# Kernel optimization log

Hardware: AMD Instinct MI355X
Metric: run time of the kernel (lower is better)

## Reference

```python
import jax, jax.numpy as jnp
import numpy as np

L = 4096   # num_tokens (one prefill sequence)
D = 2048   # hidden_size
HK = 16    # num_k_heads
HV = 32    # num_v_heads
DK = 128   # head_k_dim
DV = 128   # head_v_dim
RATIO = HV // HK
EPS = 1e-6


def setup_inputs() -> dict:
    key = jax.random.key(0)
    ks = jax.random.split(key, 11)
    s = 0.02
    return {
        "hidden_states": jax.random.normal(ks[0], (L, D), jnp.float32),
        "Wq": jax.random.normal(ks[1], (D, HK * DK), jnp.float32) * s,
        "Wk": jax.random.normal(ks[2], (D, HK * DK), jnp.float32) * s,
        "Wv": jax.random.normal(ks[3], (D, HV * DV), jnp.float32) * s,
        "Wz": jax.random.normal(ks[4], (D, HV * DV), jnp.float32) * s,
        "Wb": jax.random.normal(ks[5], (D, HV), jnp.float32) * s,
        "Wa": jax.random.normal(ks[6], (D, HV), jnp.float32) * s,
        "A_log": jnp.log(jax.random.uniform(ks[7], (HV,), jnp.float32, 1.0, 16.0)),
        "dt_bias": jax.random.normal(ks[8], (HV,), jnp.float32) * 0.5,
        "norm_weight": jnp.ones((DV,), jnp.float32),
        "W_out": jax.random.normal(ks[9], (HV * DV, D), jnp.float32) * s,
    }


def _l2norm(x):
    return x * jax.lax.rsqrt(jnp.sum(x * x, axis=-1, keepdims=True) + EPS)


def reference(hidden_states, Wq, Wk, Wv, Wz, Wb, Wa, A_log, dt_bias, norm_weight, W_out):
    h = hidden_states
    # --- input projections (qkvz + ba split) ---
    q = _l2norm((h @ Wq).reshape(L, HK, DK))            # [L, HK, DK]
    k = _l2norm((h @ Wk).reshape(L, HK, DK))
    v = (h @ Wv).reshape(L, HV, DV)                     # [L, HV, DV]
    z = (h @ Wz).reshape(L, HV, DV)                     # gate for RMSNorm
    beta = jax.nn.sigmoid(h @ Wb)                       # [L, HV]
    g = -jnp.exp(A_log) * jax.nn.softplus(h @ Wa + dt_bias)  # [L, HV]
    decay = jnp.exp(g)                                  # per-token per-head decay
    # repeat shared q/k heads to value heads (GQA ratio)
    q = jnp.repeat(q, RATIO, axis=1) * (DK ** -0.5)     # [L, HV, DK]
    k = jnp.repeat(k, RATIO, axis=1)

    # --- gated delta rule recurrence over tokens ---
    def step(S, xs):
        q_t, k_t, v_t, b_t, d_t = xs                    # [HV,DK],[HV,DK],[HV,DV],[HV],[HV]
        S = S * d_t[:, None, None]                      # decay state [HV, DK, DV]
        pred = jnp.einsum('hk,hkv->hv', k_t, S)         # memory readout
        delta = (v_t - pred) * b_t[:, None]             # delta-rule correction
        S = S + k_t[:, :, None] * delta[:, None, :]
        o = jnp.einsum('hk,hkv->hv', q_t, S)
        return S, o

    S0 = jnp.zeros((HV, DK, DV), jnp.float32)
    _, core = jax.lax.scan(step, S0, (q, k, v, beta, decay))  # core: [L, HV, DV]

    # --- gated RMSNorm: x * silu(z), rms-normalize over head dim ---
    x = core * jax.nn.silu(z)
    x = x * jax.lax.rsqrt(jnp.mean(x * x, axis=-1, keepdims=True) + EPS) * norm_weight

    # --- output projection ---
    return x.reshape(L, HV * DV) @ W_out                # [L, D]
```

## Files before the change

kernel.cpp:

```cpp
#include <hip/hip_runtime.h>

#define LTOK 4096
#define DHID 2048
#define HKN  16
#define HVN  32
#define DKK  128
#define NTOT 12288

typedef unsigned short u16;
typedef __attribute__((ext_vector_type(8))) short short8;
typedef __attribute__((ext_vector_type(8))) unsigned short u16x8;
typedef __attribute__((ext_vector_type(4))) unsigned short u16x4;
typedef __attribute__((ext_vector_type(4))) float f32x4;

__device__ __forceinline__ float b2f(u16 u) {
  unsigned int x = ((unsigned int)u) << 16;
  return __builtin_bit_cast(float, x);
}
__device__ __forceinline__ u16 f2bf(float f) {
  unsigned int u = __builtin_bit_cast(unsigned int, f);
  u += 0x7FFFu + ((u >> 16) & 1u);
  return (u16)(u >> 16);
}

template<int C> __device__ __forceinline__ float dppmv(float x) {
  int i = __builtin_amdgcn_update_dpp(0, __builtin_bit_cast(int, x), C, 0xF, 0xF, true);
  return __builtin_bit_cast(float, i);
}
__device__ __forceinline__ float red16(float x) {
  x += dppmv<0xB1>(x);
  x += dppmv<0x4E>(x);
  x += dppmv<0x124>(x);
  x += dppmv<0x128>(x);
  return x;
}

__device__ __forceinline__ void gld16(const void* g, void* l) {
  __builtin_amdgcn_global_load_lds((const __attribute__((address_space(1))) void*)g,
                                   (__attribute__((address_space(3))) void*)l, 16, 0, 0);
}

template<int OFF> __device__ __forceinline__ short8 dsr(unsigned a) {
  short8 r;
  asm volatile("ds_read_b128 %0, %1 offset:%2" : "=v"(r) : "v"(a), "n"(OFF));
  return r;
}

__device__ __forceinline__ int sw16(int r, int c, int rowc) { return (r * rowc + c) ^ ((r & 7) << 3); }

__device__ __forceinline__ void cstore(u16* C, size_t i, float v) { C[i] = f2bf(v); }
__device__ __forceinline__ void cstore(float* C, size_t i, float v) { C[i] = v; }

__global__ __launch_bounds__(256)
void k_cvt(const float* __restrict__ s, u16* __restrict__ d, int n) {
  const int i = (blockIdx.x * 256 + threadIdx.x) * 4;
  const float4 v = *(const float4*)(s + i);
  ushort4 o;
  o.x = f2bf(v.x); o.y = f2bf(v.y); o.z = f2bf(v.z); o.w = f2bf(v.w);
  *(ushort4*)(d + i) = o;
}

__global__ __launch_bounds__(256)
void k_tr(const float* __restrict__ src, u16* __restrict__ dst, int R, int C) {
  __shared__ float tl[32][33];
  const int r0 = blockIdx.y * 32, c0 = blockIdx.x * 32;
  const int tr = threadIdx.x >> 3, tc = (threadIdx.x & 7) * 4;
  const float4 v = *(const float4*)(src + (size_t)(r0 + tr) * C + c0 + tc);
  tl[tr][tc] = v.x; tl[tr][tc + 1] = v.y; tl[tr][tc + 2] = v.z; tl[tr][tc + 3] = v.w;
  __syncthreads();
  ushort4 o;
  o.x = f2bf(tl[tc + 0][tr]); o.y = f2bf(tl[tc + 1][tr]);
  o.z = f2bf(tl[tc + 2][tr]); o.w = f2bf(tl[tc + 3][tr]);
  *(ushort4*)(dst + (size_t)(c0 + tr) * R + r0 + tc) = o;
}

#define MFMA16(a, b, c) __builtin_amdgcn_mfma_f32_16x16x32_bf16(a, b, c, 0, 0, 0)

template<typename OutT, int NWN>
__global__ __launch_bounds__(512, 2)
void k_g256(const u16* __restrict__ A, const u16* __restrict__ Bt, OutT* __restrict__ C,
            int M, int N, int K, int NT) {
  constexpr int BUFE = 8192 + NWN * 2048;
  constexpr int BN = NWN * 64;
  __shared__ u16 Lds[4 * BUFE];
  const int tid = threadIdx.x;
  const int lane = tid & 63, w = tid >> 6;
  const int fr = lane & 15, fq = lane >> 4;
  const int wm = (w >> 2) * 128, wn = (w & 3) * (NWN * 16);
  const int nkt = K >> 5;
  const size_t sK = (size_t)K;

  const int MT = gridDim.x / NT;
  const int nts = (NT < 16) ? NT : 16;
  const int per_super = MT * nts;
  const int super = blockIdx.x / per_super;
  const int within = blockIdx.x % per_super;
  const int mtg = MT >> 3;
  const int q = within >> 3;
  const int mt = (within & 7) * mtg + (q % mtg);
  const int nt = super * nts + q / mtg;

  const int kslot = ((tid & 3) ^ ((tid >> 3) & 3)) * 8;
  const u16* aS = A + (size_t)(mt * 256 + (tid >> 2)) * sK + kslot;
  const u16* bS = Bt + (size_t)(nt * BN + (tid >> 2)) * sK + kslot;

  f32x4 acc[8][NWN] = {};

  auto STAGE = [&](int kt_) {
    const int sk = (kt_ < nkt) ? kt_ : nkt - 1;
    u16* base = &Lds[(kt_ & 3) * BUFE];
    gld16(aS + (size_t)sk * 32, base + w * 512);
    gld16(aS + 128 * sK + (size_t)sk * 32, base + w * 512 + 4096);
    gld16(bS + (size_t)sk * 32, base + 8192 + w * 512);
    if constexpr (NWN == 4)
      gld16(bS + 128 * sK + (size_t)sk * 32, base + 8192 + w * 512 + 4096);
  };

  STAGE(0); STAGE(1); STAGE(2);

  const int akey = (fr >> 1) & 3;
  const unsigned ldsBase = (unsigned)(size_t)(__attribute__((address_space(3))) void*)&Lds[0];
  const unsigned aA0 = ldsBase + 2u * (unsigned)((wm + fr) * 32 + ((fq ^ akey) << 3));
  const unsigned bA0 = ldsBase + 2u * (unsigned)(8192 + (wn + fr) * 32 + ((fq ^ akey) << 3));

  short8 afA[8], bfA[NWN], afB[8], bfB[NWN];

#define RD(afX, bfX, kt_) {                                                   \
    const unsigned bo = (unsigned)(((kt_) & 3) * BUFE * 2);                   \
    const unsigned aAr = aA0 + bo, bAr = bA0 + bo;                            \
    bfX[0] = dsr<0>(bAr); bfX[1] = dsr<1024>(bAr);                            \
    if constexpr (NWN == 4) { bfX[2] = dsr<2048>(bAr); bfX[3] = dsr<3072>(bAr); } \
    afX[0] = dsr<0>(aAr);    afX[1] = dsr<1024>(aAr);                         \
    afX[2] = dsr<2048>(aAr); afX[3] = dsr<3072>(aAr);                         \
    afX[4] = dsr<4096>(aAr); afX[5] = dsr<5120>(aAr);                         \
    afX[6] = dsr<6144>(aAr); afX[7] = dsr<7168>(aAr); }

  if constexpr (NWN == 4) asm volatile("s_waitcnt vmcnt(8)" ::: "memory");
  else                    asm volatile("s_waitcnt vmcnt(6)" ::: "memory");
  __builtin_amdgcn_s_barrier();
  RD(afA, bfA, 0)
  asm volatile("s_waitcnt lgkmcnt(0)" ::: "memory");
  __builtin_amdgcn_sched_barrier(0);

#define ITER(kt_, afC, bfC, afN, bfN) {                                       \
    STAGE((kt_) + 3);                                                         \
    if constexpr (NWN == 4) asm volatile("s_waitcnt vmcnt(8)" ::: "memory");  \
    else                    asm volatile("s_waitcnt vmcnt(6)" ::: "memory");  \
    __builtin_amdgcn_s_barrier();                                             \
    __builtin_amdgcn_sched_barrier(0);                                        \
    RD(afN, bfN, (kt_) + 1)                                                   \
    __builtin_amdgcn_sched_barrier(0);                                        \
    __builtin_amdgcn_s_setprio(1);                                            \
    _Pragma("unroll")                                                         \
    for (int i = 0; i < 8; ++i)                                               \
      _Pragma("unroll")                                                       \
      for (int j = 0; j < NWN; ++j)                                           \
        acc[i][j] = MFMA16(afC[i], bfC[j], acc[i][j]);                        \
    __builtin_amdgcn_s_setprio(0);                                            \
    asm volatile("s_waitcnt lgkmcnt(0)" ::: "memory");                        \
    __builtin_amdgcn_sched_barrier(0); }

  for (int kt = 0; kt < nkt; kt += 2) {
    ITER(kt, afA, bfA, afB, bfB)
    ITER(kt + 1, afB, bfB, afA, bfA)
  }
#undef ITER
#undef RD

  const int r0 = mt * 256 + wm + fq * 4;
  const int c0 = nt * BN + wn + fr;
#pragma unroll
  for (int i = 0; i < 8; ++i)
#pragma unroll
    for (int j = 0; j < NWN; ++j)
#pragma unroll
      for (int e = 0; e < 4; ++e)
        cstore(C, (size_t)(r0 + i * 16 + e) * N + c0 + j * 16, acc[i][j][e]);
}

__global__ __launch_bounds__(256)
void k_ba(const float* __restrict__ h, const float* __restrict__ Wb, const float* __restrict__ Wa,
          const float* __restrict__ A_log, const float* __restrict__ dtb,
          float* __restrict__ beta, float* __restrict__ g_out) {
  const int w = threadIdx.x >> 6, lane = threadIdx.x & 63;
  const int t = blockIdx.x * 4 + w;
  const int j = lane & 31;
  const bool isB = lane < 32;
  const float* __restrict__ hr = h + (size_t)t * DHID;
  const float* Wc = isB ? Wb : Wa;
  float acc = 0.f;
  for (int kk = 0; kk < DHID; ++kk) acc = fmaf(hr[kk], Wc[(size_t)kk * HVN + j], acc);
  if (isB) {
    beta[(size_t)t * HVN + j] = 1.f / (1.f + expf(-acc));
  } else {
    float xx = acc + dtb[j];
    float sp = (xx > 20.f) ? xx : log1pf(expf(xx));
    g_out[(size_t)t * HVN + j] = -expf(A_log[j]) * sp;
  }
}

__global__ __launch_bounds__(256)
void k_l2n(u16* __restrict__ qkvz) {
  const int w = threadIdx.x >> 6, lane = threadIdx.x & 63;
  const int r = blockIdx.x * 4 + w;
  const int isK = r >> 16;
  const int rr = r & 65535;
  const int t = rr >> 4, hd = rr & 15;
  u16* p = qkvz + (size_t)t * NTOT + isK * 2048 + hd * DKK + lane * 2;
  float a = b2f(p[0]), b = b2f(p[1]);
  float ss = a * a + b * b;
  ss = red16(ss);
  ss += __shfl_xor(ss, 16);
  ss += __shfl_xor(ss, 32);
  const float sc = rsqrtf(ss + 1e-6f) * (isK ? 1.f : 0.08838834764831845f);
  p[0] = f2bf(a * sc); p[1] = f2bf(b * sc);
}

__global__ __launch_bounds__(256)
void k_r1(const u16* __restrict__ qkvz, const float* __restrict__ beta_g,
          const float* __restrict__ g_g, u16* __restrict__ UM_g, float* __restrict__ cumL_g) {
  const int pair = blockIdx.x;
  const int hv = pair >> 6, n = pair & 63;
  const int hk = hv >> 1;
  const int t0 = n * 64;
  const int tid = threadIdx.x, lane = tid & 63, wv = tid >> 6;
  const int fr = lane & 15, fq = lane >> 4;

  __shared__ __align__(16) u16 Xb[256 * 64];
  __shared__ __align__(16) u16 Dbuf0[64 * 64 * 2];
  __shared__ __align__(16) u16 Dbuf1[64 * 64 * 2];
  __shared__ float Lc[64];
  __shared__ float Bc[64];
  u16* Kl = Dbuf0;

  const int j = tid & 63, h = tid >> 6;
  const u16* kg = qkvz + (size_t)(t0 + j) * NTOT + 2048 + hk * DKK + h * 32;
  const u16* vg = qkvz + (size_t)(t0 + j) * NTOT + 4096 + hv * DKK + h * 32;
  u16x8 kv[4], vv[4];
#pragma unroll
  for (int i = 0; i < 4; ++i) { kv[i] = *(const u16x8*)(kg + i * 8); vv[i] = *(const u16x8*)(vg + i * 8); }
  if (tid < 64) {
    Lc[tid] = g_g[(size_t)(t0 + tid) * HVN + hv];
    Bc[tid] = beta_g[(size_t)(t0 + tid) * HVN + hv];
  }
#pragma unroll
  for (int i = 0; i < 4; ++i) *(u16x8*)&Kl[sw16(j, h * 32 + i * 8, 128)] = kv[i];
  __syncthreads();
  if (tid == 0) { float a = 0.f; for (int t = 0; t < 64; ++t) { a += Lc[t]; Lc[t] = a; } }
  __syncthreads();
  if (tid < 64) cumL_g[(size_t)pair * 64 + tid] = Lc[tid];

  {
    const float bj = Bc[j];
    const float mj = bj * __expf(Lc[j]);
#pragma unroll
    for (int i = 0; i < 4; ++i)
#pragma unroll
      for (int e = 0; e < 8; ++e) {
        int c = h * 32 + i * 8 + e;
        Xb[sw16(c, j, 64)] = f2bf(bj * b2f(vv[i][e]));
        Xb[sw16(128 + c, j, 64)] = f2bf(mj * b2f(kv[i][e]));
      }
  }
  f32x4 kk[4] = {};
#pragma unroll
  for (int ks = 0; ks < 4; ++ks) {
    short8 afr = *(const short8*)&Kl[sw16(wv * 16 + fr, ks * 32 + fq * 8, 128)];
#pragma unroll
    for (int ct = 0; ct < 4; ++ct) {
      short8 bfr = *(const short8*)&Kl[sw16(ct * 16 + fr, ks * 32 + fq * 8, 128)];
      kk[ct] = MFMA16(afr, bfr, kk[ct]);
    }
  }
  __syncthreads();

  f32x4 acc[16];
#pragma unroll
  for (int ct = 0; ct < 16; ++ct) {
    u16x4 xi = *(const u16x4*)&Xb[sw16(ct * 16 + fr, wv * 16 + fq * 4, 64)];
    acc[ct][0] = b2f(xi[0]); acc[ct][1] = b2f(xi[1]); acc[ct][2] = b2f(xi[2]); acc[ct][3] = b2f(xi[3]);
  }
#pragma unroll
  for (int ct = 0; ct < 4; ++ct) {
    const int s = ct * 16 + fr;
    u16x4 pk;
#pragma unroll
    for (int e = 0; e < 4; ++e) {
      const int t = wv * 16 + fq * 4 + e;
      float v = (s < t) ? -Bc[t] * __expf(Lc[t] - Lc[s]) * kk[ct][e] : 0.f;
      pk[e] = f2bf(v);
      Dbuf0[sw16(t, s, 64)] = pk[e];
    }
    *(u16x4*)&Dbuf0[4096 + sw16(s, wv * 16 + fq * 4, 64)] = pk;
  }
  __syncthreads();

  u16* DA = Dbuf0;
  u16* DB = Dbuf1;
  for (int stg = 0; stg < 6; ++stg) {
    u16* Dr = DA;
    u16* Dc = DA + 4096;
    short8 da0 = *(const short8*)&Dr[sw16(wv * 16 + fr, 0 + fq * 8, 64)];
    short8 da1 = *(const short8*)&Dr[sw16(wv * 16 + fr, 32 + fq * 8, 64)];
#pragma unroll
    for (int ct = 0; ct < 16; ++ct) {
      short8 b0 = *(const short8*)&Xb[sw16(ct * 16 + fr, 0 + fq * 8, 64)];
      short8 b1 = *(const short8*)&Xb[sw16(ct * 16 + fr, 32 + fq * 8, 64)];
      acc[ct] = MFMA16(da0, b0, acc[ct]);
      acc[ct] = MFMA16(da1, b1, acc[ct]);
    }
    f32x4 sq[4] = {};
    if (stg < 5) {
#pragma unroll
      for (int ct = 0; ct < 4; ++ct) {
        short8 sb0 = *(const short8*)&Dc[sw16(ct * 16 + fr, 0 + fq * 8, 64)];
        short8 sb1 = *(const short8*)&Dc[sw16(ct * 16 + fr, 32 + fq * 8, 64)];
        sq[ct] = MFMA16(da0, sb0, sq[ct]);
        sq[ct] = MFMA16(da1, sb1, sq[ct]);
      }
    }
    __syncthreads();
#pragma unroll
    for (int ct = 0; ct < 16; ++ct) {
      u16x4 pk;
      pk[0] = f2bf(acc[ct][0]); pk[1] = f2bf(acc[ct][1]); pk[2] = f2bf(acc[ct][2]); pk[3] = f2bf(acc[ct][3]);
      *(u16x4*)&Xb[sw16(ct * 16 + fr, wv * 16 + fq * 4, 64)] = pk;
    }
    if (stg < 5) {
#pragma unroll
      for (int ct = 0; ct < 4; ++ct) {
        u16x4 pk;
        pk[0] = f2bf(sq[ct][0]); pk[1] = f2bf(sq[ct][1]); pk[2] = f2bf(sq[ct][2]); pk[3] = f2bf(sq[ct][3]);
        *(u16x4*)&(DB + 4096)[sw16(ct * 16 + fr, wv * 16 + fq * 4, 64)] = pk;
#pragma unroll
        for (int e = 0; e < 4; ++e) DB[sw16(wv * 16 + fq * 4 + e, ct * 16 + fr, 64)] = pk[e];
      }
    }
    __syncthreads();
    u16* tmp = DA; DA = DB; DB = tmp;
  }

#pragma unroll
  for (int ct = 0; ct < 16; ++ct) {
    const int c = ct * 16 + fr;
#pragma unroll
    for (int e = 0; e < 4; ++e) {
      const int t = wv * 16 + fq * 4 + e;
      float v = acc[ct][e];
      if (ct >= 8) v = -v;
      UM_g[((size_t)pair * 64 + t) * 256 + c] = f2bf(v);
    }
  }
}

__global__ __launch_bounds__(512)
void k_r2(u16* __restrict__ qkvz, const u16* __restrict__ UM_g,
          const float* __restrict__ cumL_g, u16* __restrict__ o1_g) {
  const int hv = blockIdx.x >> 2, cs = blockIdx.x & 3;
  const int hk = hv >> 1;
  const int tid = threadIdx.x, lane = tid & 63, w = tid >> 6;
  const int fr = lane & 15, fq = lane >> 4;
  const int j = tid & 63, h = tid >> 6;
  const int tw = w & 3, dwv = w >> 2;

  __shared__ __align__(16) u16 Ml2[2][8192];
  __shared__ __align__(16) u16 Ql2[2][8192];
  __shared__ __align__(16) u16 Kt2[2][8192];
  __shared__ __align__(16) u16 dT[2048];
  __shared__ __align__(16) u16 SbT[4096];
  __shared__ __align__(16) u16 o1b[2048];
  __shared__ float Lc2[2][64];

  f32x4 sacc[2];
#pragma unroll
  for (int d = 0; d < 2; ++d) sacc[d] = (f32x4){0.f, 0.f, 0.f, 0.f};
  for (int i = tid; i < 4096; i += 512) SbT[i] = 0;

  u16x8 pQ0, pQ1, pK0, pK1, pM0, pM1;
  u16 pUn0, pUn1, pUn2, pUn3, pUc0, pUc1, pUc2, pUc3;
  float pL, pL63;

#define PREF(nn) {                                                            \
    const int nc = ((nn) < 64) ? (nn) : 63;                                   \
    const int pr = hv * 64 + nc; const int tt0 = nc * 64;                     \
    const u16* qg = qkvz + (size_t)(tt0 + j) * NTOT + hk * DKK + h * 16;      \
    pQ0 = *(const u16x8*)qg;          pQ1 = *(const u16x8*)(qg + 8);          \
    pK0 = *(const u16x8*)(qg + 2048); pK1 = *(const u16x8*)(qg + 2056);       \
    const u16* mg = UM_g + ((size_t)pr * 64 + j) * 256;                       \
    pM0 = *(const u16x8*)(mg + 128 + h * 16);                                 \
    pM1 = *(const u16x8*)(mg + 136 + h * 16);                                 \
    const u16* ug = UM_g + ((size_t)pr * 64 + tw * 16 + fq * 4) * 256         \
                    + cs * 32 + dwv * 16 + fr;                                \
    pUn0 = ug[0]; pUn1 = ug[256]; pUn2 = ug[512]; pUn3 = ug[768];             \
    pL = cumL_g[(size_t)pr * 64 + j]; pL63 = cumL_g[(size_t)pr * 64 + 63]; }

#define STW(b) {                                                              \
    *(u16x8*)&Ql2[b][sw16(j, h * 16, 128)] = pQ0;                             \
    *(u16x8*)&Ql2[b][sw16(j, h * 16 + 8, 128)] = pQ1;                         \
    *(u16x8*)&Ml2[b][sw16(j, h * 16, 128)] = pM0;                             \
    *(u16x8*)&Ml2[b][sw16(j, h * 16 + 8, 128)] = pM1;                         \
    const float scK = __expf(pL63 - pL);                                      \
    _Pragma("unroll")                                                         \
    for (int e = 0; e < 8; ++e) {                                             \
      Kt2[b][sw16(h * 16 + e, j, 64)] = f2bf(scK * b2f(pK0[e]));              \
      Kt2[b][sw16(h * 16 + 8 + e, j, 64)] = f2bf(scK * b2f(pK1[e]));          \
    }                                                                         \
    if (h == 0) Lc2[b][j] = pL; }

  PREF(0)
  STW(0)
  __syncthreads();

  for (int n = 0; n < 64; ++n) {
    const int cur = n & 1;
    const int pair = hv * 64 + n, t0 = n * 64;
    pUc0 = pUn0; pUc1 = pUn1; pUc2 = pUn2; pUc3 = pUn3;
    const float curL63 = pL63;
    PREF(n + 1)

    short8 amf[4], aqf[4];
#pragma unroll
    for (int ks = 0; ks < 4; ++ks) {
      amf[ks] = *(const short8*)&Ml2[cur][sw16(tw * 16 + fr, ks * 32 + fq * 8, 128)];
      aqf[ks] = *(const short8*)&Ql2[cur][sw16(tw * 16 + fr, ks * 32 + fq * 8, 128)];
    }
    float el[4];
#pragma unroll
    for (int e = 0; e < 4; ++e) el[e] = __expf(Lc2[cur][tw * 16 + fq * 4 + e]);
    {
      f32x4 dc;
      dc[0] = b2f(pUc0); dc[1] = b2f(pUc1); dc[2] = b2f(pUc2); dc[3] = b2f(pUc3);
      f32x4 oc = {};
#pragma unroll
      for (int ks = 0; ks < 4; ++ks) {
        short8 bs = *(const short8*)&SbT[sw16(dwv * 16 + fr, ks * 32 + fq * 8, 128)];
        dc = MFMA16(amf[ks], bs, dc);
        oc = MFMA16(aqf[ks], bs, oc);
      }
      u16x4 pkd;
      pkd[0] = f2bf(dc[0]); pkd[1] = f2bf(dc[1]); pkd[2] = f2bf(dc[2]); pkd[3] = f2bf(dc[3]);
      *(u16x4*)&dT[sw16(dwv * 16 + fr, tw * 16 + fq * 4, 64)] = pkd;
      u16x4 pko;
#pragma unroll
      for (int e = 0; e < 4; ++e) pko[e] = f2bf(oc[e] * el[e]);
      *(u16x4*)&o1b[sw16(dwv * 16 + fr, tw * 16 + fq * 4, 64)] = pko;
    }
    __syncthreads();

    {
      const int i = tid * 4;
      u16x4 vd = *(const u16x4*)&dT[i];
      const int f = cs * 2048 + i;
      *(u16x4*)(qkvz + (size_t)(t0 + (f >> 7)) * NTOT + 4096 + hv * DKK + (f & 127)) = vd;
      u16x4 vo = *(const u16x4*)&o1b[i];
      *(u16x4*)(o1_g + (size_t)pair * 8192 + cs * 2048 + i) = vo;
    }
    STW(cur ^ 1)
    {
      const float eC = __expf(curL63);
      short8 ak0 = *(const short8*)&Kt2[cur][sw16(w * 16 + fr, fq * 8, 64)];
      short8 ak1 = *(const short8*)&Kt2[cur][sw16(w * 16 + fr, 32 + fq * 8, 64)];
#pragma unroll
      for (int d = 0; d < 2; ++d) {
        short8 bd0 = *(const short8*)&dT[sw16(d * 16 + fr, fq * 8, 64)];
        short8 bd1 = *(const short8*)&dT[sw16(d * 16 + fr, 32 + fq * 8, 64)];
        f32x4 sa = sacc[d];
#pragma unroll
        for (int e = 0; e < 4; ++e) sa[e] *= eC;
        sa = MFMA16(ak0, bd0, sa);
        sa = MFMA16(ak1, bd1, sa);
        sacc[d] = sa;
        u16x4 pk;
        pk[0] = f2bf(sa[0]); pk[1] = f2bf(sa[1]); pk[2] = f2bf(sa[2]); pk[3] = f2bf(sa[3]);
        *(u16x4*)&SbT[sw16(d * 16 + fr, w * 16 + fq * 4, 128)] = pk;
      }
    }
    __syncthreads();
  }
#undef PREF
#undef STW
}

__global__ __launch_bounds__(512)
void k_r3(const u16* __restrict__ qkvz, const u16* __restrict__ o1_g,
          const float* __restrict__ cumL_g, const float* __restrict__ nw,
          u16* __restrict__ x) {
  const int pair = blockIdx.x, hv = pair >> 6, n = pair & 63, hk = hv >> 1, t0 = n * 64;
  const int tid = threadIdx.x, lane = tid & 63, w = tid >> 6;
  const int fr = lane & 15, fq = lane >> 4;
  const int j = tid & 63, h = tid >> 6;

  __shared__ __align__(16) u16 Ql[8192];
  __shared__ __align__(16) u16 Kl[8192];
  __shared__ __align__(16) u16 Gl[4096];
  __shared__ __align__(16) u16 dTl[8192];
  __shared__ __align__(16) u16 o1l[8192];
  __shared__ __align__(16) float of[64 * 132];
  __shared__ float Lc[64];
  __shared__ float Lw[128];

  {
    const u16* qg = qkvz + (size_t)(t0 + j) * NTOT + hk * DKK + h * 16;
    u16x8 q0 = *(const u16x8*)qg, q1 = *(const u16x8*)(qg + 8);
    u16x8 k0 = *(const u16x8*)(qg + 2048), k1 = *(const u16x8*)(qg + 2056);
    *(u16x8*)&Ql[sw16(j, h * 16, 128)] = q0;
    *(u16x8*)&Ql[sw16(j, h * 16 + 8, 128)] = q1;
    *(u16x8*)&Kl[sw16(j, h * 16, 128)] = k0;
    *(u16x8*)&Kl[sw16(j, h * 16 + 8, 128)] = k1;
  }
#pragma unroll
  for (int it = 0; it < 2; ++it) {
    const int f = ((w * 2 + it) * 64 + lane) * 8;
    gld16(qkvz + (size_t)(t0 + (f >> 7)) * NTOT + 4096 + hv * DKK + (f & 127),
          (char*)dTl + (w * 2 + it) * 1024);
    gld16(o1_g + (size_t)pair * 8192 + f, (char*)o1l + (w * 2 + it) * 1024);
  }
  if (tid < 64) Lc[tid] = cumL_g[(size_t)pair * 64 + tid];
  if (tid < 128) Lw[tid] = nw[tid];
  __syncthreads();

  const int tw = w & 3, sp = (w >> 2) * 2;
  {
    f32x4 kk0 = {}, kk1 = {};
#pragma unroll
    for (int ks = 0; ks < 4; ++ks) {
      short8 aq = *(const short8*)&Ql[sw16(tw * 16 + fr, ks * 32 + fq * 8, 128)];
      short8 b0 = *(const short8*)&Kl[sw16(sp * 16 + fr, ks * 32 + fq * 8, 128)];
      short8 b1 = *(const short8*)&Kl[sw16((sp + 1) * 16 + fr, ks * 32 + fq * 8, 128)];
      kk0 = MFMA16(aq, b0, kk0);
      kk1 = MFMA16(aq, b1, kk1);
    }
#pragma unroll
    for (int e = 0; e < 4; ++e) {
      const int t = tw * 16 + fq * 4 + e;
      const float Lt = Lc[t];
      const int s0 = sp * 16 + fr, s1 = s0 + 16;
      Gl[sw16(t, s0, 64)] = f2bf((s0 <= t) ? kk0[e] * __expf(Lt - Lc[s0]) : 0.f);
      Gl[sw16(t, s1, 64)] = f2bf((s1 <= t) ? kk1[e] * __expf(Lt - Lc[s1]) : 0.f);
    }
  }
  __syncthreads();

  {
    short8 ag0 = *(const short8*)&Gl[sw16(tw * 16 + fr, fq * 8, 64)];
    short8 ag1 = *(const short8*)&Gl[sw16(tw * 16 + fr, 32 + fq * 8, 64)];
#pragma unroll
    for (int dd = 0; dd < 4; ++dd) {
      const int d = (w >> 2) * 4 + dd;
      short8 bd0 = *(const short8*)&dTl[sw16(d * 16 + fr, fq * 8, 64)];
      short8 bd1 = *(const short8*)&dTl[sw16(d * 16 + fr, 32 + fq * 8, 64)];
      f32x4 oc = {};
      oc = MFMA16(ag0, bd0, oc);
      oc = MFMA16(ag1, bd1, oc);
#pragma unroll
      for (int e = 0; e < 4; ++e) of[(tw * 16 + fq * 4 + e) * 132 + d * 16 + fr] = oc[e];
    }
  }
  __syncthreads();

  {
    const int t = tid >> 3, q8 = tid & 7;
    const u16* zp = qkvz + (size_t)(t0 + t) * NTOT + 8192 + hv * DKK + q8 * 16;
    float xv[16];
    float ss = 0.f;
#pragma unroll
    for (int i = 0; i < 2; ++i) {
      u16x8 zv = *(const u16x8*)(zp + i * 8);
#pragma unroll
      for (int e = 0; e < 8; ++e) {
        const int dv = q8 * 16 + i * 8 + e;
        float z = b2f(zv[e]);
        float o = of[t * 132 + dv] + b2f(o1l[sw16(dv, t, 64)]);
        float xx = o * (z / (1.f + __expf(-z)));
        xv[i * 8 + e] = xx;
        ss = fmaf(xx, xx, ss);
      }
    }
    ss += __shfl_xor(ss, 1);
    ss += __shfl_xor(ss, 2);
    ss += __shfl_xor(ss, 4);
    const float scl = rsqrtf(ss * (1.f / 128.f) + 1e-6f);
    u16* xo = x + (size_t)(t0 + t) * 4096 + hv * DKK + q8 * 16;
#pragma unroll
    for (int i = 0; i < 2; ++i) {
      u16x8 pk;
#pragma unroll
      for (int e = 0; e < 8; ++e) pk[e] = f2bf(xv[i * 8 + e] * scl * Lw[q8 * 16 + i * 8 + e]);
      *(u16x8*)(xo + i * 8) = pk;
    }
  }
}

extern "C" void kernel_launch(void* const* d_in, const int* in_sizes, int n_in,
                              void* d_out, int out_size, void* d_ws, size_t ws_size,
                              hipStream_t stream) {
  const float* h    = (const float*)d_in[0];
  const float* Wq   = (const float*)d_in[1];
  const float* Wk   = (const float*)d_in[2];
  const float* Wv   = (const float*)d_in[3];
  const float* Wz   = (const float*)d_in[4];
  const float* Wb   = (const float*)d_in[5];
  const float* Wa   = (const float*)d_in[6];
  const float* Alog = (const float*)d_in[7];
  const float* dtb  = (const float*)d_in[8];
  const float* nw   = (const float*)d_in[9];
  const float* Wo   = (const float*)d_in[10];
  char* ws = (char*)d_ws;
  u16* h_bf  = (u16*)(ws);
  u16* Wt    = (u16*)(ws + 16777216ull);
  u16* UM    = (u16*)(ws);
  u16* Wto   = (u16*)(ws + 67108864ull);
  u16* qkvz  = (u16*)(ws + 83886080ull);
  u16* o1g   = (u16*)(ws + 184549376ull);
  u16* xbuf  = (u16*)(ws + 16777216ull);
  float* beta  = (float*)(ws + 218103808ull);
  float* g     = (float*)(ws + 218103808ull + 524288ull);
  float* cumL  = (float*)(ws + 218103808ull + 1048576ull);

  k_cvt<<<8192, 256, 0, stream>>>(h, h_bf, LTOK * DHID);
  k_tr<<<dim3(64, 64), 256, 0, stream>>>(Wq, Wt, 2048, 2048);
  k_tr<<<dim3(64, 64), 256, 0, stream>>>(Wk, Wt + 2048ull * 2048, 2048, 2048);
  k_tr<<<dim3(128, 64), 256, 0, stream>>>(Wv, Wt + 4096ull * 2048, 2048, 4096);
  k_tr<<<dim3(128, 64), 256, 0, stream>>>(Wz, Wt + 8192ull * 2048, 2048, 4096);
  k_tr<<<dim3(64, 128), 256, 0, stream>>>(Wo, Wto, 4096, 2048);
  k_g256<u16, 4><<<768, 512, 0, stream>>>(h_bf, Wt, qkvz, 4096, 12288, 2048, 48);
  k_ba<<<1024, 256, 0, stream>>>(h, Wb, Wa, Alog, dtb, beta, g);
  k_l2n<<<32768, 256, 0, stream>>>(qkvz);
  k_r1<<<2048, 256, 0, stream>>>(qkvz, beta, g, UM, cumL);
  k_r2<<<128, 512, 0, stream>>>(qkvz, UM, cumL, o1g);
  k_r3<<<2048, 512, 0, stream>>>(qkvz, o1g, cumL, nw, xbuf);
  k_g256<float, 2><<<256, 512, 0, stream>>>(xbuf, Wto, (float*)d_out, 4096, 2048, 4096, 16);
}
```

Baseline: 818.0 us.

## Pre-pack weights into MFMA fragment layout and load B directly to registers

```diff
diff --git a/kernel.cpp b/kernel.cpp
--- a/kernel.cpp
+++ b/kernel.cpp
@@ -45,6 +45,12 @@
   asm volatile("ds_read_b128 %0, %1 offset:%2" : "=v"(r) : "v"(a), "n"(OFF));
   return r;
 }
+__device__ __forceinline__ short8 gldx4(const u16* p) {
+  short8 r;
+  asm volatile("global_load_dwordx4 %0, %1, off" : "=v"(r) : "v"(p));
+  return r;
+}
+#define KEEPV(x) asm volatile("" :: "v"(x))
 
 __device__ __forceinline__ int sw16(int r, int c, int rowc) { return (r * rowc + c) ^ ((r & 7) << 3); }
 
@@ -61,28 +67,26 @@
 }
 
 __global__ __launch_bounds__(256)
-void k_tr(const float* __restrict__ src, u16* __restrict__ dst, int R, int C) {
-  __shared__ float tl[32][33];
-  const int r0 = blockIdx.y * 32, c0 = blockIdx.x * 32;
-  const int tr = threadIdx.x >> 3, tc = (threadIdx.x & 7) * 4;
-  const float4 v = *(const float4*)(src + (size_t)(r0 + tr) * C + c0 + tc);
-  tl[tr][tc] = v.x; tl[tr][tc + 1] = v.y; tl[tr][tc + 2] = v.z; tl[tr][tc + 3] = v.w;
-  __syncthreads();
-  ushort4 o;
-  o.x = f2bf(tl[tc + 0][tr]); o.y = f2bf(tl[tc + 1][tr]);
-  o.z = f2bf(tl[tc + 2][tr]); o.w = f2bf(tl[tc + 3][tr]);
-  *(ushort4*)(dst + (size_t)(c0 + tr) * R + r0 + tc) = o;
+void k_trf(const float* __restrict__ W, u16* __restrict__ Bf, int Ncols, int nkt, int j16base) {
+  const int wv = threadIdx.x >> 6, lane = threadIdx.x & 63;
+  const int frag = blockIdx.x * 4 + wv;
+  const int j16 = frag / nkt, kt = frag % nkt;
+  const int r0 = kt * 32 + (lane >> 4) * 8;
+  const int c = j16 * 16 + (lane & 15);
+  u16x8 o;
+#pragma unroll
+  for (int e = 0; e < 8; ++e) o[e] = f2bf(W[(size_t)(r0 + e) * Ncols + c]);
+  *(u16x8*)(Bf + ((size_t)(j16base + j16) * nkt + kt) * 512 + lane * 8) = o;
 }
 
 #define MFMA16(a, b, c) __builtin_amdgcn_mfma_f32_16x16x32_bf16(a, b, c, 0, 0, 0)
 
 template<typename OutT, int NWN>
 __global__ __launch_bounds__(512, 2)
-void k_g256(const u16* __restrict__ A, const u16* __restrict__ Bt, OutT* __restrict__ C,
+void k_g256(const u16* __restrict__ A, const u16* __restrict__ Bf, OutT* __restrict__ C,
             int M, int N, int K, int NT) {
-  constexpr int BUFE = 8192 + NWN * 2048;
   constexpr int BN = NWN * 64;
-  __shared__ u16 Lds[4 * BUFE];
+  __shared__ u16 Lds[4 * 8192];
   const int tid = threadIdx.x;
   const int lane = tid & 63, w = tid >> 6;
   const int fr = lane & 15, fq = lane >> 4;
@@ -102,70 +106,80 @@
 
   const int kslot = ((tid & 3) ^ ((tid >> 3) & 3)) * 8;
   const u16* aS = A + (size_t)(mt * 256 + (tid >> 2)) * sK + kslot;
-  const u16* bS = Bt + (size_t)(nt * BN + (tid >> 2)) * sK + kslot;
+
+  const int jw = nt * (BN / 16) + (w & 3) * NWN;
+  const u16* bp[NWN];
+#pragma unroll
+  for (int j = 0; j < NWN; ++j) bp[j] = Bf + ((size_t)(jw + j) * nkt) * 512 + lane * 8;
 
   f32x4 acc[8][NWN] = {};
 
   auto STAGE = [&](int kt_) {
     const int sk = (kt_ < nkt) ? kt_ : nkt - 1;
-    u16* base = &Lds[(kt_ & 3) * BUFE];
+    u16* base = &Lds[(kt_ & 3) * 8192];
     gld16(aS + (size_t)sk * 32, base + w * 512);
     gld16(aS + 128 * sK + (size_t)sk * 32, base + w * 512 + 4096);
-    gld16(bS + (size_t)sk * 32, base + 8192 + w * 512);
-    if constexpr (NWN == 4)
-      gld16(bS + 128 * sK + (size_t)sk * 32, base + 8192 + w * 512 + 4096);
   };
 
-  STAGE(0); STAGE(1); STAGE(2);
+#define LOADB(bset, kt_) {                                                    \
+    const int sk2 = ((kt_) < nkt) ? (kt_) : (nkt - 1);                        \
+    _Pragma("unroll")                                                         \
+    for (int j = 0; j < NWN; ++j) bset[j] = gldx4(bp[j] + (size_t)sk2 * 512); }
 
   const int akey = (fr >> 1) & 3;
   const unsigned ldsBase = (unsigned)(size_t)(__attribute__((address_space(3))) void*)&Lds[0];
   const unsigned aA0 = ldsBase + 2u * (unsigned)((wm + fr) * 32 + ((fq ^ akey) << 3));
-  const unsigned bA0 = ldsBase + 2u * (unsigned)(8192 + (wn + fr) * 32 + ((fq ^ akey) << 3));
-
-  short8 afA[8], bfA[NWN], afB[8], bfB[NWN];
-
-#define RD(afX, bfX, kt_) {                                                   \
-    const unsigned bo = (unsigned)(((kt_) & 3) * BUFE * 2);                   \
-    const unsigned aAr = aA0 + bo, bAr = bA0 + bo;                            \
-    bfX[0] = dsr<0>(bAr); bfX[1] = dsr<1024>(bAr);                            \
-    if constexpr (NWN == 4) { bfX[2] = dsr<2048>(bAr); bfX[3] = dsr<3072>(bAr); } \
+
+  short8 afA[8], afB[8], bs0[NWN], bs1[NWN];
+
+#define RD(afX, kt_) {                                                        \
+    const unsigned aAr = aA0 + (unsigned)(((kt_) & 3) * 16384);               \
     afX[0] = dsr<0>(aAr);    afX[1] = dsr<1024>(aAr);                         \
     afX[2] = dsr<2048>(aAr); afX[3] = dsr<3072>(aAr);                         \
     afX[4] = dsr<4096>(aAr); afX[5] = dsr<5120>(aAr);                         \
     afX[6] = dsr<6144>(aAr); afX[7] = dsr<7168>(aAr); }
 
-  if constexpr (NWN == 4) asm volatile("s_waitcnt vmcnt(8)" ::: "memory");
-  else                    asm volatile("s_waitcnt vmcnt(6)" ::: "memory");
+  STAGE(0); STAGE(1); STAGE(2);
+  LOADB(bs0, 0)
+  asm volatile("s_waitcnt vmcnt(0)" ::: "memory");
   __builtin_amdgcn_s_barrier();
-  RD(afA, bfA, 0)
+  RD(afA, 0)
   asm volatile("s_waitcnt lgkmcnt(0)" ::: "memory");
   __builtin_amdgcn_sched_barrier(0);
 
-#define ITER(kt_, afC, bfC, afN, bfN) {                                       \
+#define ITER(kt_, afC, bC, afN, bN) {                                         \
+    LOADB(bN, (kt_) + 1)                                                      \
     STAGE((kt_) + 3);                                                         \
     if constexpr (NWN == 4) asm volatile("s_waitcnt vmcnt(8)" ::: "memory");  \
     else                    asm volatile("s_waitcnt vmcnt(6)" ::: "memory");  \
     __builtin_amdgcn_s_barrier();                                             \
     __builtin_amdgcn_sched_barrier(0);                                        \
-    RD(afN, bfN, (kt_) + 1)                                                   \
+    RD(afN, (kt_) + 1)                                                        \
     __builtin_amdgcn_sched_barrier(0);                                        \
     __builtin_amdgcn_s_setprio(1);                                            \
     _Pragma("unroll")                                                         \
     for (int i = 0; i < 8; ++i)                                               \
       _Pragma("unroll")                                                       \
       for (int j = 0; j < NWN; ++j)                                           \
-        acc[i][j] = MFMA16(afC[i], bfC[j], acc[i][j]);                        \
+        acc[i][j] = MFMA16(afC[i], bC[j], acc[i][j]);                         \
     __builtin_amdgcn_s_setprio(0);                                            \
     asm volatile("s_waitcnt lgkmcnt(0)" ::: "memory");                        \
     __builtin_amdgcn_sched_barrier(0); }
 
   for (int kt = 0; kt < nkt; kt += 2) {
-    ITER(kt, afA, bfA, afB, bfB)
-    ITER(kt + 1, afB, bfB, afA, bfA)
+    ITER(kt, afA, bs0, afB, bs1)
+    ITER(kt + 1, afB, bs1, afA, bs0)
   }
 #undef ITER
 #undef RD
+#undef LOADB
+
+  asm volatile("s_waitcnt vmcnt(0) lgkmcnt(0)" ::: "memory");
+  __builtin_amdgcn_sched_barrier(0);
+  KEEPV(bs0[0]); KEEPV(bs0[1]);
+  if constexpr (NWN == 4) { KEEPV(bs0[2]); KEEPV(bs0[3]); }
+  KEEPV(afA[0]); KEEPV(afA[1]); KEEPV(afA[2]); KEEPV(afA[3]);
+  KEEPV(afA[4]); KEEPV(afA[5]); KEEPV(afA[6]); KEEPV(afA[7]);
 
   const int r0 = mt * 256 + wm + fq * 4;
   const int c0 = nt * BN + wn + fr;
@@ -607,9 +621,9 @@
   const float* Wo   = (const float*)d_in[10];
   char* ws = (char*)d_ws;
   u16* h_bf  = (u16*)(ws);
-  u16* Wt    = (u16*)(ws + 16777216ull);
+  u16* Bfq   = (u16*)(ws + 16777216ull);
   u16* UM    = (u16*)(ws);
-  u16* Wto   = (u16*)(ws + 67108864ull);
+  u16* Bfo   = (u16*)(ws + 67108864ull);
   u16* qkvz  = (u16*)(ws + 83886080ull);
   u16* o1g   = (u16*)(ws + 184549376ull);
   u16* xbuf  = (u16*)(ws + 16777216ull);
@@ -618,16 +632,16 @@
   float* cumL  = (float*)(ws + 218103808ull + 1048576ull);
 
   k_cvt<<<8192, 256, 0, stream>>>(h, h_bf, LTOK * DHID);
-  k_tr<<<dim3(64, 64), 256, 0, stream>>>(Wq, Wt, 2048, 2048);
-  k_tr<<<dim3(64, 64), 256, 0, stream>>>(Wk, Wt + 2048ull * 2048, 2048, 2048);
-  k_tr<<<dim3(128, 64), 256, 0, stream>>>(Wv, Wt + 4096ull * 2048, 2048, 4096);
-  k_tr<<<dim3(128, 64), 256, 0, stream>>>(Wz, Wt + 8192ull * 2048, 2048, 4096);
-  k_tr<<<dim3(64, 128), 256, 0, stream>>>(Wo, Wto, 4096, 2048);
-  k_g256<u16, 4><<<768, 512, 0, stream>>>(h_bf, Wt, qkvz, 4096, 12288, 2048, 48);
+  k_trf<<<2048, 256, 0, stream>>>(Wq, Bfq, 2048, 64, 0);
+  k_trf<<<2048, 256, 0, stream>>>(Wk, Bfq, 2048, 64, 128);
+  k_trf<<<4096, 256, 0, stream>>>(Wv, Bfq, 4096, 64, 256);
+  k_trf<<<4096, 256, 0, stream>>>(Wz, Bfq, 4096, 64, 512);
+  k_trf<<<4096, 256, 0, stream>>>(Wo, Bfo, 2048, 128, 0);
+  k_g256<u16, 4><<<768, 512, 0, stream>>>(h_bf, Bfq, qkvz, 4096, 12288, 2048, 48);
   k_ba<<<1024, 256, 0, stream>>>(h, Wb, Wa, Alog, dtb, beta, g);
   k_l2n<<<32768, 256, 0, stream>>>(qkvz);
   k_r1<<<2048, 256, 0, stream>>>(qkvz, beta, g, UM, cumL);
   k_r2<<<128, 512, 0, stream>>>(qkvz, UM, cumL, o1g);
   k_r3<<<2048, 512, 0, stream>>>(qkvz, o1g, cumL, nw, xbuf);
-  k_g256<float, 2><<<256, 512, 0, stream>>>(xbuf, Wto, (float*)d_out, 4096, 2048, 4096, 16);
-}
+  k_g256<float, 2><<<256, 512, 0, stream>>>(xbuf, Bfo, (float*)d_out, 4096, 2048, 4096, 16);
+}
```

After: 811.6 us. No clear change (-0.8%).
